# Optimization experiments

Measured on AMD Instinct MI355X. Metric: run time of the kernel, lower is better.

Reference implementation:

```python
import jax, jax.numpy as jnp
import numpy as np

RES, GATE, SKIP, K, DIL, CIN = 128, 256, 128, 3, 2, 80
PAD = (K - 1) * DIL


def _wn(v, g):
    # weight_norm: w = g * v / ||v||, norm over all dims except dim 0 (out_channels)
    norm = jnp.sqrt(jnp.sum(v * v, axis=(1, 2), keepdims=True))
    return v * (g.reshape(-1, 1, 1) / norm)


def setup_inputs() -> dict:
    key = jax.random.key(0)
    ks = jax.random.split(key, 12)
    s = lambda *sh: 1.0 / np.sqrt(np.prod(sh[1:]))
    d = {
        "x": jax.random.normal(ks[0], (8, RES, 32768), dtype=jnp.float32),
        "condition": jax.random.normal(ks[1], (8, CIN, 32768), dtype=jnp.float32),
        "conv_v": jax.random.normal(ks[2], (GATE, RES, K), dtype=jnp.float32) * s(GATE, RES, K),
        "conv_g": jnp.ones((GATE,), dtype=jnp.float32),
        "conv_b": jnp.zeros((GATE,), dtype=jnp.float32),
        "lc_v": jax.random.normal(ks[3], (GATE, CIN, 1), dtype=jnp.float32) * s(GATE, CIN, 1),
        "lc_g": jnp.ones((GATE,), dtype=jnp.float32),
        "skip_v": jax.random.normal(ks[4], (SKIP, GATE // 2, 1), dtype=jnp.float32) * s(SKIP, GATE // 2, 1),
        "skip_g": jnp.ones((SKIP,), dtype=jnp.float32),
        "skip_b": jnp.zeros((SKIP,), dtype=jnp.float32),
        "out_v": jax.random.normal(ks[5], (RES, GATE // 2, 1), dtype=jnp.float32) * s(RES, GATE // 2, 1),
        "out_g": jnp.ones((RES,), dtype=jnp.float32),
        "out_b": jnp.zeros((RES,), dtype=jnp.float32),
    }
    return d


def reference(x, condition, conv_v, conv_g, conv_b, lc_v, lc_g,
              skip_v, skip_g, skip_b, out_v, out_g, out_b):
    residual = x
    w = _wn(conv_v, conv_g)  # [GATE, RES, K]
    # torch pads symmetrically then slices [:, :, :-PAD]; equivalent to left-only pad
    h = jax.lax.conv_general_dilated(
        x, w, window_strides=(1,), padding=[(PAD, 0)], rhs_dilation=(DIL,),
        dimension_numbers=("NCH", "OIH", "NCH"))
    h = h + conv_b[None, :, None]  # [B, GATE, T]
    a, b = jnp.split(h, 2, axis=1)
    lc_w = _wn(lc_v, lc_g)[:, :, 0]  # [GATE, CIN]
    c = jnp.einsum("oc,bct->bot", lc_w, condition)
    ca, cb = jnp.split(c, 2, axis=1)
    g = jnp.tanh(a + ca) * jax.nn.sigmoid(b + cb)  # [B, GATE//2, T]
    skip_w = _wn(skip_v, skip_g)[:, :, 0]
    s = jnp.einsum("oc,bct->bot", skip_w, g) + skip_b[None, :, None]
    out_w = _wn(out_v, out_g)[:, :, 0]
    o = jnp.einsum("oc,bct->bot", out_w, g) + out_b[None, :, None]
    return (o + residual, s)
```

## Files before the change

### kernel.cpp

```cpp
#include <hip/hip_runtime.h>
#include <hip/hip_bf16.h>

#define B_N   8
#define T_N   32768
#define RESC  128
#define GATEC 256
#define CINC  80
#define CINP  96
#define NT    64
#define HALO  4
#define XROWS 68
#define XSTR  136
#define CSTR  96
#define HSTR  136

#define AP1_ELEMS (16*12*512)
#define AP2_ELEMS (16*3*512)
#define AP3_ELEMS (16*4*512)

#define OFF_S ((size_t)B_N * RESC * T_N)

typedef __attribute__((ext_vector_type(8))) short short8;
typedef __attribute__((ext_vector_type(4))) float f32x4;

__device__ __forceinline__ ushort f2bf(float f) {
  union { float f; unsigned int u; } c; c.f = f;
  unsigned int u = c.u;
  u += 0x7fffu + ((u >> 16) & 1u);
  return (ushort)(u >> 16);
}
__device__ __forceinline__ float bf2f(ushort s) {
  union { unsigned int u; float f; } c; c.u = ((unsigned int)s) << 16;
  return c.f;
}

__global__ __launch_bounds__(256) void wn_pack_kernel(
    const float* __restrict__ conv_v, const float* __restrict__ conv_g,
    const float* __restrict__ lc_v,  const float* __restrict__ lc_g,
    const float* __restrict__ skip_v,const float* __restrict__ skip_g,
    const float* __restrict__ out_v, const float* __restrict__ out_g,
    ushort* __restrict__ Ap1, ushort* __restrict__ Ap2, ushort* __restrict__ Ap3) {
  const int o   = blockIdx.x;
  const int tid = threadIdx.x;
  const int mtg = o >> 4, r = o & 15;
  __shared__ float red[256];

  float s = 0.f;
  for (int e = tid; e < RESC * 3; e += 256) { float v = conv_v[o * RESC * 3 + e]; s += v * v; }
  red[tid] = s; __syncthreads();
  for (int off = 128; off > 0; off >>= 1) { if (tid < off) red[tid] += red[tid + off]; __syncthreads(); }
  const float csc = conv_g[o] / sqrtf(red[0]);
  __syncthreads();
  for (int e = tid; e < 384; e += 256) {
    const int ks = e >> 5, q = (e >> 3) & 3, j = e & 7;
    const int tap = ks >> 2, ci = (ks & 3) * 32 + q * 8 + j;
    Ap1[((mtg * 12 + ks) * 64 + q * 16 + r) * 8 + j] = f2bf(conv_v[(o * RESC + ci) * 3 + tap] * csc);
  }

  s = 0.f;
  for (int e = tid; e < CINC; e += 256) { float v = lc_v[o * CINC + e]; s += v * v; }
  red[tid] = s; __syncthreads();
  for (int off = 128; off > 0; off >>= 1) { if (tid < off) red[tid] += red[tid + off]; __syncthreads(); }
  const float lsc = lc_g[o] / sqrtf(red[0]);
  __syncthreads();
  for (int e = tid; e < CINP; e += 256) {
    const int ks = e >> 5, q = (e >> 3) & 3, j = e & 7;
    const float wv = (e < CINC) ? lc_v[o * CINC + e] * lsc : 0.f;
    Ap2[((mtg * 3 + ks) * 64 + q * 16 + r) * 8 + j] = f2bf(wv);
  }

  const float* vrow = (o < 128) ? (skip_v + o * 128) : (out_v + (o - 128) * 128);
  const float  gg   = (o < 128) ? skip_g[o] : out_g[o - 128];
  s = 0.f;
  for (int e = tid; e < 128; e += 256) { float v = vrow[e]; s += v * v; }
  red[tid] = s; __syncthreads();
  for (int off = 128; off > 0; off >>= 1) { if (tid < off) red[tid] += red[tid + off]; __syncthreads(); }
  const float ssc = gg / sqrtf(red[0]);
  for (int e = tid; e < 128; e += 256) {
    const int ks = e >> 5, q = (e >> 3) & 3, j = e & 7;
    Ap3[((mtg * 4 + ks) * 64 + q * 16 + r) * 8 + j] = f2bf(vrow[e] * ssc);
  }
}

__global__ __launch_bounds__(256) void fused_block_kernel(
    const float* __restrict__ x, const float* __restrict__ cond,
    const float* __restrict__ conv_b, const float* __restrict__ skip_b,
    const float* __restrict__ out_b,
    const ushort* __restrict__ Ap1, const ushort* __restrict__ Ap2,
    const ushort* __restrict__ Ap3,
    float* __restrict__ out) {
  const int tid  = threadIdx.x;
  const int w    = tid >> 6;
  const int lane = tid & 63;
  const int q    = lane >> 4;
  const int n    = lane & 15;
  const int blk  = blockIdx.x;
  const int b    = blk >> 9;
  const int t0   = (blk & 511) << 6;

  __shared__ ushort smem[17408];
  ushort* xs  = smem;
  ushort* cs  = smem + XROWS * XSTR;
  ushort* hsA = smem;
  ushort* hsB = smem + NT * HSTR;

  {
    const int g4 = tid >> 3;
    const int c0 = g4 << 2;
    const int tt = (tid & 7) << 3;
    const float* xp = x + ((size_t)b * RESC + c0) * T_N + t0 + tt;
    float va[4][8];
#pragma unroll
    for (int rr = 0; rr < 4; ++rr) {
      const float4* rp = (const float4*)(xp + (size_t)rr * T_N);
      const float4 a0 = rp[0], a1 = rp[1];
      va[rr][0] = a0.x; va[rr][1] = a0.y; va[rr][2] = a0.z; va[rr][3] = a0.w;
      va[rr][4] = a1.x; va[rr][5] = a1.y; va[rr][6] = a1.z; va[rr][7] = a1.w;
    }
#pragma unroll
    for (int ss = 0; ss < 8; ++ss) {
      const unsigned lo = (unsigned)f2bf(va[0][ss]) | ((unsigned)f2bf(va[1][ss]) << 16);
      const unsigned hi = (unsigned)f2bf(va[2][ss]) | ((unsigned)f2bf(va[3][ss]) << 16);
      *(uint2*)&xs[(HALO + tt + ss) * XSTR + c0] = make_uint2(lo, hi);
    }
  }
  if (tid < RESC) {
    float h0 = 0.f, h1 = 0.f, h2 = 0.f, h3 = 0.f;
    if (t0 > 0) {
      const float4 hv = *(const float4*)(x + ((size_t)b * RESC + tid) * T_N + t0 - 4);
      h0 = hv.x; h1 = hv.y; h2 = hv.z; h3 = hv.w;
    }
    xs[0 * XSTR + tid] = f2bf(h0);
    xs[1 * XSTR + tid] = f2bf(h1);
    xs[2 * XSTR + tid] = f2bf(h2);
    xs[3 * XSTR + tid] = f2bf(h3);
  }
  if (tid < 160) {
    const int g4 = tid >> 3;
    const int c0 = g4 << 2;
    const int tt = (tid & 7) << 3;
    const float* cp = cond + ((size_t)b * CINC + c0) * T_N + t0 + tt;
    float va[4][8];
#pragma unroll
    for (int rr = 0; rr < 4; ++rr) {
      const float4* rp = (const float4*)(cp + (size_t)rr * T_N);
      const float4 a0 = rp[0], a1 = rp[1];
      va[rr][0] = a0.x; va[rr][1] = a0.y; va[rr][2] = a0.z; va[rr][3] = a0.w;
      va[rr][4] = a1.x; va[rr][5] = a1.y; va[rr][6] = a1.z; va[rr][7] = a1.w;
    }
#pragma unroll
    for (int ss = 0; ss < 8; ++ss) {
      const unsigned lo = (unsigned)f2bf(va[0][ss]) | ((unsigned)f2bf(va[1][ss]) << 16);
      const unsigned hi = (unsigned)f2bf(va[2][ss]) | ((unsigned)f2bf(va[3][ss]) << 16);
      *(uint2*)&cs[(tt + ss) * CSTR + c0] = make_uint2(lo, hi);
    }
  } else {
    const int e0 = tid - 160;
    for (int z = e0; z < 512; z += 96) {
      const int t = z >> 3, cp2 = z & 7;
      *(unsigned int*)&cs[t * CSTR + CINC + cp2 * 2] = 0u;
    }
  }
  __syncthreads();

  f32x4 acc[4][4];
#pragma unroll
  for (int mt = 0; mt < 4; ++mt) {
    const float4 cb = *(const float4*)(conv_b + w * 64 + mt * 16 + q * 4);
#pragma unroll
    for (int nt = 0; nt < 4; ++nt) acc[mt][nt] = (f32x4){cb.x, cb.y, cb.z, cb.w};
  }
#pragma unroll
  for (int ks = 0; ks < 12; ++ks) {
    const int tap = ks >> 2;
    const int cb2 = (ks & 3) << 5;
    short8 af[4], bfr[4];
#pragma unroll
    for (int mt = 0; mt < 4; ++mt)
      af[mt] = *(const short8*)(Ap1 + ((w * 4 + mt) * 12 + ks) * 512 + lane * 8);
#pragma unroll
    for (int nt = 0; nt < 4; ++nt)
      bfr[nt] = *(const short8*)&xs[(nt * 16 + n + tap * 2) * XSTR + cb2 + q * 8];
#pragma unroll
    for (int mt = 0; mt < 4; ++mt)
#pragma unroll
      for (int nt = 0; nt < 4; ++nt)
        acc[mt][nt] = __builtin_amdgcn_mfma_f32_16x16x32_bf16(af[mt], bfr[nt], acc[mt][nt], 0, 0, 0);
  }
#pragma unroll
  for (int ks = 0; ks < 3; ++ks) {
    short8 af[4], bfr[4];
#pragma unroll
    for (int mt = 0; mt < 4; ++mt)
      af[mt] = *(const short8*)(Ap2 + ((w * 4 + mt) * 3 + ks) * 512 + lane * 8);
#pragma unroll
    for (int nt = 0; nt < 4; ++nt)
      bfr[nt] = *(const short8*)&cs[(nt * 16 + n) * CSTR + ks * 32 + q * 8];
#pragma unroll
    for (int mt = 0; mt < 4; ++mt)
#pragma unroll
      for (int nt = 0; nt < 4; ++nt)
        acc[mt][nt] = __builtin_amdgcn_mfma_f32_16x16x32_bf16(af[mt], bfr[nt], acc[mt][nt], 0, 0, 0);
  }
  __syncthreads();

  const int colbase = (w & 1) << 6;
  {
    ushort* hdst = (w < 2) ? hsA : hsB;
#pragma unroll
    for (int mt = 0; mt < 4; ++mt)
#pragma unroll
      for (int nt = 0; nt < 4; ++nt) {
        const f32x4 v = acc[mt][nt];
        float r0, r1, r2, r3;
        if (w < 2) {
          r0 = 1.f - 2.f / (__expf(2.f * v[0]) + 1.f);
          r1 = 1.f - 2.f / (__expf(2.f * v[1]) + 1.f);
          r2 = 1.f - 2.f / (__expf(2.f * v[2]) + 1.f);
          r3 = 1.f - 2.f / (__expf(2.f * v[3]) + 1.f);
        } else {
          r0 = 1.f / (1.f + __expf(-v[0]));
          r1 = 1.f / (1.f + __expf(-v[1]));
          r2 = 1.f / (1.f + __expf(-v[2]));
          r3 = 1.f / (1.f + __expf(-v[3]));
        }
        const unsigned lo = (unsigned)f2bf(r0) | ((unsigned)f2bf(r1) << 16);
        const unsigned hi = (unsigned)f2bf(r2) | ((unsigned)f2bf(r3) << 16);
        *(uint2*)&hdst[(nt * 16 + n) * HSTR + colbase + mt * 16 + q * 4] = make_uint2(lo, hi);
      }
  }
  __syncthreads();

  {
    const int prow = tid >> 2;
    const int pc0  = (tid & 3) << 5;
#pragma unroll
    for (int s2 = 0; s2 < 8; ++s2) {
      const int col = pc0 + (s2 << 2);
      const uint2 ua = *(uint2*)&hsA[prow * HSTR + col];
      const uint2 ub = *(uint2*)&hsB[prow * HSTR + col];
      const float a0 = bf2f((ushort)ua.x), a1 = bf2f((ushort)(ua.x >> 16));
      const float a2 = bf2f((ushort)ua.y), a3 = bf2f((ushort)(ua.y >> 16));
      const float b0 = bf2f((ushort)ub.x), b1 = bf2f((ushort)(ub.x >> 16));
      const float b2 = bf2f((ushort)ub.y), b3 = bf2f((ushort)(ub.y >> 16));
      const unsigned lo = (unsigned)f2bf(a0 * b0) | ((unsigned)f2bf(a1 * b1) << 16);
      const unsigned hi = (unsigned)f2bf(a2 * b2) | ((unsigned)f2bf(a3 * b3) << 16);
      *(uint2*)&hsA[prow * HSTR + col] = make_uint2(lo, hi);
    }
  }
  __syncthreads();

  {
    const float* bias = (w < 2) ? skip_b : out_b;
#pragma unroll
    for (int mt = 0; mt < 4; ++mt) {
      const float4 bb = *(const float4*)(bias + colbase + mt * 16 + q * 4);
#pragma unroll
      for (int nt = 0; nt < 4; ++nt) acc[mt][nt] = (f32x4){bb.x, bb.y, bb.z, bb.w};
    }
#pragma unroll
    for (int ks = 0; ks < 4; ++ks) {
      short8 af[4], bfr[4];
#pragma unroll
      for (int mt = 0; mt < 4; ++mt)
        af[mt] = *(const short8*)(Ap3 + ((w * 4 + mt) * 4 + ks) * 512 + lane * 8);
#pragma unroll
      for (int nt = 0; nt < 4; ++nt)
        bfr[nt] = *(const short8*)&hsA[(nt * 16 + n) * HSTR + ks * 32 + q * 8];
#pragma unroll
      for (int mt = 0; mt < 4; ++mt)
#pragma unroll
        for (int nt = 0; nt < 4; ++nt)
          acc[mt][nt] = __builtin_amdgcn_mfma_f32_16x16x32_bf16(af[mt], bfr[nt], acc[mt][nt], 0, 0, 0);
    }
  }

#pragma unroll
  for (int mt = 0; mt < 4; ++mt)
#pragma unroll
    for (int nt = 0; nt < 4; ++nt) {
      const int ch = colbase + mt * 16 + q * 4;
      const int t  = t0 + nt * 16 + n;
      const f32x4 v = acc[mt][nt];
      if (w < 2) {
        float* dst = out + OFF_S + ((size_t)(b * RESC + ch)) * T_N + t;
#pragma unroll
        for (int i = 0; i < 4; ++i) dst[(size_t)i * T_N] = v[i];
      } else {
        const float* xr = x + ((size_t)(b * RESC + ch)) * T_N + t;
        float* dst = out + ((size_t)(b * RESC + ch)) * T_N + t;
#pragma unroll
        for (int i = 0; i < 4; ++i) dst[(size_t)i * T_N] = v[i] + xr[(size_t)i * T_N];
      }
    }
}

extern "C" void kernel_launch(void* const* d_in, const int* in_sizes, int n_in,
                              void* d_out, int out_size, void* d_ws, size_t ws_size,
                              hipStream_t stream) {
  const float* x      = (const float*)d_in[0];
  const float* cond   = (const float*)d_in[1];
  const float* conv_v = (const float*)d_in[2];
  const float* conv_g = (const float*)d_in[3];
  const float* conv_b = (const float*)d_in[4];
  const float* lc_v   = (const float*)d_in[5];
  const float* lc_g   = (const float*)d_in[6];
  const float* skip_v = (const float*)d_in[7];
  const float* skip_g = (const float*)d_in[8];
  const float* skip_b = (const float*)d_in[9];
  const float* out_v  = (const float*)d_in[10];
  const float* out_g  = (const float*)d_in[11];
  const float* out_b  = (const float*)d_in[12];

  ushort* Ap1 = (ushort*)d_ws;
  ushort* Ap2 = Ap1 + AP1_ELEMS;
  ushort* Ap3 = Ap2 + AP2_ELEMS;

  hipLaunchKernelGGL(wn_pack_kernel, dim3(256), dim3(256), 0, stream,
                     conv_v, conv_g, lc_v, lc_g, skip_v, skip_g, out_v, out_g,
                     Ap1, Ap2, Ap3);
  hipLaunchKernelGGL(fused_block_kernel, dim3(4096), dim3(256), 0, stream,
                     x, cond, conv_b, skip_b, out_b, Ap1, Ap2, Ap3, (float*)d_out);
}
```

Baseline: 509.4 us.

## Gate tanh/sigmoid in registers and swap operands for time-contiguous output stores

Each wave now computes matching tanh and sigmoid channel halves (aa/ab accumulators) so the gate product is formed in registers. This removes the separate shared-memory elementwise multiply pass and one barrier. The final GEMM swaps operand roles so each lane holds four consecutive time steps, which allows float4 global stores and residual loads instead of strided scalar accesses. Input staging is reorganized to use packed bf16 conversion with 16-byte LDS stores, and the shared-memory footprint is reduced. The cost is some added address arithmetic.

```diff
diff --git a/kernel.cpp b/kernel.cpp
--- a/kernel.cpp
+++ b/kernel.cpp
@@ -6,13 +6,11 @@
 #define RESC  128
 #define GATEC 256
 #define CINC  80
-#define CINP  96
 #define NT    64
 #define HALO  4
 #define XROWS 68
 #define XSTR  136
-#define CSTR  96
-#define HSTR  136
+#define CSTR  104
 
 #define AP1_ELEMS (16*12*512)
 #define AP2_ELEMS (16*3*512)
@@ -29,9 +27,9 @@
   u += 0x7fffu + ((u >> 16) & 1u);
   return (ushort)(u >> 16);
 }
-__device__ __forceinline__ float bf2f(ushort s) {
-  union { unsigned int u; float f; } c; c.u = ((unsigned int)s) << 16;
-  return c.f;
+__device__ __forceinline__ unsigned pkbf(float a, float b) {
+  __hip_bfloat162 h = __float22bfloat162_rn(float2{a, b});
+  unsigned u; __builtin_memcpy(&u, &h, 4); return u;
 }
 
 __global__ __launch_bounds__(256) void wn_pack_kernel(
@@ -63,7 +61,7 @@
   for (int off = 128; off > 0; off >>= 1) { if (tid < off) red[tid] += red[tid + off]; __syncthreads(); }
   const float lsc = lc_g[o] / sqrtf(red[0]);
   __syncthreads();
-  for (int e = tid; e < CINP; e += 256) {
+  for (int e = tid; e < 96; e += 256) {
     const int ks = e >> 5, q = (e >> 3) & 3, j = e & 7;
     const float wv = (e < CINC) ? lc_v[o * CINC + e] * lsc : 0.f;
     Ap2[((mtg * 3 + ks) * 64 + q * 16 + r) * 8 + j] = f2bf(wv);
@@ -98,30 +96,27 @@
   const int b    = blk >> 9;
   const int t0   = (blk & 511) << 6;
 
-  __shared__ ushort smem[17408];
-  ushort* xs  = smem;
-  ushort* cs  = smem + XROWS * XSTR;
-  ushort* hsA = smem;
-  ushort* hsB = smem + NT * HSTR;
+  __shared__ ushort smem[XROWS * XSTR + NT * CSTR];
+  ushort* xs = smem;
+  ushort* cs = smem + XROWS * XSTR;
+  ushort* gs = smem;
 
   {
-    const int g4 = tid >> 3;
-    const int c0 = g4 << 2;
-    const int tt = (tid & 7) << 3;
+    const int c0 = (tid & 15) << 3;
+    const int tt = (tid >> 4) << 2;
     const float* xp = x + ((size_t)b * RESC + c0) * T_N + t0 + tt;
-    float va[4][8];
-#pragma unroll
-    for (int rr = 0; rr < 4; ++rr) {
-      const float4* rp = (const float4*)(xp + (size_t)rr * T_N);
-      const float4 a0 = rp[0], a1 = rp[1];
-      va[rr][0] = a0.x; va[rr][1] = a0.y; va[rr][2] = a0.z; va[rr][3] = a0.w;
-      va[rr][4] = a1.x; va[rr][5] = a1.y; va[rr][6] = a1.z; va[rr][7] = a1.w;
-    }
-#pragma unroll
-    for (int ss = 0; ss < 8; ++ss) {
-      const unsigned lo = (unsigned)f2bf(va[0][ss]) | ((unsigned)f2bf(va[1][ss]) << 16);
-      const unsigned hi = (unsigned)f2bf(va[2][ss]) | ((unsigned)f2bf(va[3][ss]) << 16);
-      *(uint2*)&xs[(HALO + tt + ss) * XSTR + c0] = make_uint2(lo, hi);
+    float4 va[8];
+#pragma unroll
+    for (int rr = 0; rr < 8; ++rr) va[rr] = *(const float4*)(xp + (size_t)rr * T_N);
+    const float* vf = (const float*)va;
+#pragma unroll
+    for (int i = 0; i < 4; ++i) {
+      uint4 pkd;
+      pkd.x = pkbf(vf[0 * 4 + i], vf[1 * 4 + i]);
+      pkd.y = pkbf(vf[2 * 4 + i], vf[3 * 4 + i]);
+      pkd.z = pkbf(vf[4 * 4 + i], vf[5 * 4 + i]);
+      pkd.w = pkbf(vf[6 * 4 + i], vf[7 * 4 + i]);
+      *(uint4*)&xs[(HALO + tt + i) * XSTR + c0] = pkd;
     }
   }
   if (tid < RESC) {
@@ -135,164 +130,148 @@
     xs[2 * XSTR + tid] = f2bf(h2);
     xs[3 * XSTR + tid] = f2bf(h3);
   }
-  if (tid < 160) {
-    const int g4 = tid >> 3;
-    const int c0 = g4 << 2;
-    const int tt = (tid & 7) << 3;
-    const float* cp = cond + ((size_t)b * CINC + c0) * T_N + t0 + tt;
-    float va[4][8];
-#pragma unroll
-    for (int rr = 0; rr < 4; ++rr) {
-      const float4* rp = (const float4*)(cp + (size_t)rr * T_N);
-      const float4 a0 = rp[0], a1 = rp[1];
-      va[rr][0] = a0.x; va[rr][1] = a0.y; va[rr][2] = a0.z; va[rr][3] = a0.w;
-      va[rr][4] = a1.x; va[rr][5] = a1.y; va[rr][6] = a1.z; va[rr][7] = a1.w;
-    }
-#pragma unroll
-    for (int ss = 0; ss < 8; ++ss) {
-      const unsigned lo = (unsigned)f2bf(va[0][ss]) | ((unsigned)f2bf(va[1][ss]) << 16);
-      const unsigned hi = (unsigned)f2bf(va[2][ss]) | ((unsigned)f2bf(va[3][ss]) << 16);
-      *(uint2*)&cs[(tt + ss) * CSTR + c0] = make_uint2(lo, hi);
-    }
-  } else {
-    const int e0 = tid - 160;
-    for (int z = e0; z < 512; z += 96) {
-      const int t = z >> 3, cp2 = z & 7;
-      *(unsigned int*)&cs[t * CSTR + CINC + cp2 * 2] = 0u;
-    }
-  }
-  __syncthreads();
-
-  f32x4 acc[4][4];
-#pragma unroll
-  for (int mt = 0; mt < 4; ++mt) {
-    const float4 cb = *(const float4*)(conv_b + w * 64 + mt * 16 + q * 4);
-#pragma unroll
-    for (int nt = 0; nt < 4; ++nt) acc[mt][nt] = (f32x4){cb.x, cb.y, cb.z, cb.w};
+  if (tid < 192) {
+    const int cb = tid % 12;
+    const int tq = tid / 12;
+    const int c0 = cb << 3;
+    const int tt = tq << 2;
+    if (cb < 10) {
+      const float* cp = cond + ((size_t)b * CINC + c0) * T_N + t0 + tt;
+      float4 va[8];
+#pragma unroll
+      for (int rr = 0; rr < 8; ++rr) va[rr] = *(const float4*)(cp + (size_t)rr * T_N);
+      const float* vf = (const float*)va;
+#pragma unroll
+      for (int i = 0; i < 4; ++i) {
+        uint4 pkd;
+        pkd.x = pkbf(vf[0 * 4 + i], vf[1 * 4 + i]);
+        pkd.y = pkbf(vf[2 * 4 + i], vf[3 * 4 + i]);
+        pkd.z = pkbf(vf[4 * 4 + i], vf[5 * 4 + i]);
+        pkd.w = pkbf(vf[6 * 4 + i], vf[7 * 4 + i]);
+        *(uint4*)&cs[(tt + i) * CSTR + c0] = pkd;
+      }
+    } else {
+#pragma unroll
+      for (int i = 0; i < 4; ++i)
+        *(uint4*)&cs[(tt + i) * CSTR + c0] = make_uint4(0, 0, 0, 0);
+    }
+  }
+  __syncthreads();
+
+  f32x4 aa[2][4], ab[2][4];
+#pragma unroll
+  for (int mt = 0; mt < 2; ++mt) {
+    const float4 ca = *(const float4*)(conv_b + w * 32 + mt * 16 + q * 4);
+    const float4 cb2 = *(const float4*)(conv_b + 128 + w * 32 + mt * 16 + q * 4);
+#pragma unroll
+    for (int nt = 0; nt < 4; ++nt) {
+      aa[mt][nt] = (f32x4){ca.x, ca.y, ca.z, ca.w};
+      ab[mt][nt] = (f32x4){cb2.x, cb2.y, cb2.z, cb2.w};
+    }
   }
 #pragma unroll
   for (int ks = 0; ks < 12; ++ks) {
     const int tap = ks >> 2;
-    const int cb2 = (ks & 3) << 5;
-    short8 af[4], bfr[4];
+    const int kc  = (ks & 3) << 5;
+    short8 afa[2], afb[2], bfr[4];
+#pragma unroll
+    for (int mt = 0; mt < 2; ++mt) {
+      afa[mt] = *(const short8*)(Ap1 + (((w * 2 + mt) * 12 + ks) << 9) + lane * 8);
+      afb[mt] = *(const short8*)(Ap1 + (((8 + w * 2 + mt) * 12 + ks) << 9) + lane * 8);
+    }
+#pragma unroll
+    for (int nt = 0; nt < 4; ++nt)
+      bfr[nt] = *(const short8*)&xs[(nt * 16 + n + tap * 2) * XSTR + kc + q * 8];
+#pragma unroll
+    for (int mt = 0; mt < 2; ++mt)
+#pragma unroll
+      for (int nt = 0; nt < 4; ++nt) {
+        aa[mt][nt] = __builtin_amdgcn_mfma_f32_16x16x32_bf16(afa[mt], bfr[nt], aa[mt][nt], 0, 0, 0);
+        ab[mt][nt] = __builtin_amdgcn_mfma_f32_16x16x32_bf16(afb[mt], bfr[nt], ab[mt][nt], 0, 0, 0);
+      }
+  }
+#pragma unroll
+  for (int ks = 0; ks < 3; ++ks) {
+    short8 afa[2], afb[2], bfr[4];
+#pragma unroll
+    for (int mt = 0; mt < 2; ++mt) {
+      afa[mt] = *(const short8*)(Ap2 + (((w * 2 + mt) * 3 + ks) << 9) + lane * 8);
+      afb[mt] = *(const short8*)(Ap2 + (((8 + w * 2 + mt) * 3 + ks) << 9) + lane * 8);
+    }
+#pragma unroll
+    for (int nt = 0; nt < 4; ++nt)
+      bfr[nt] = *(const short8*)&cs[(nt * 16 + n) * CSTR + (ks << 5) + q * 8];
+#pragma unroll
+    for (int mt = 0; mt < 2; ++mt)
+#pragma unroll
+      for (int nt = 0; nt < 4; ++nt) {
+        aa[mt][nt] = __builtin_amdgcn_mfma_f32_16x16x32_bf16(afa[mt], bfr[nt], aa[mt][nt], 0, 0, 0);
+        ab[mt][nt] = __builtin_amdgcn_mfma_f32_16x16x32_bf16(afb[mt], bfr[nt], ab[mt][nt], 0, 0, 0);
+      }
+  }
+  __syncthreads();
+
+#pragma unroll
+  for (int mt = 0; mt < 2; ++mt)
+#pragma unroll
+    for (int nt = 0; nt < 4; ++nt) {
+      const f32x4 va_ = aa[mt][nt];
+      const f32x4 vb_ = ab[mt][nt];
+      float g4[4];
+#pragma unroll
+      for (int i = 0; i < 4; ++i) {
+        const float th = 1.f - 2.f / (__expf(2.f * va_[i]) + 1.f);
+        const float sg = 1.f / (1.f + __expf(-vb_[i]));
+        g4[i] = th * sg;
+      }
+      const uint2 pkd = make_uint2(pkbf(g4[0], g4[1]), pkbf(g4[2], g4[3]));
+      *(uint2*)&gs[(nt * 16 + n) * XSTR + w * 32 + mt * 16 + q * 4] = pkd;
+    }
+  __syncthreads();
+
+  {
+    const int chbase = (w & 1) << 6;
+    const float* bias = (w < 2) ? skip_b : out_b;
+    f32x4 acc[4][4];
+#pragma unroll
+    for (int nt = 0; nt < 4; ++nt) {
+      const float bv = bias[chbase + nt * 16 + n];
+#pragma unroll
+      for (int mt = 0; mt < 4; ++mt) acc[mt][nt] = (f32x4){bv, bv, bv, bv};
+    }
+#pragma unroll
+    for (int ks = 0; ks < 4; ++ks) {
+      short8 ag[4], bw[4];
+#pragma unroll
+      for (int mt = 0; mt < 4; ++mt)
+        ag[mt] = *(const short8*)&gs[(mt * 16 + n) * XSTR + (ks << 5) + q * 8];
+#pragma unroll
+      for (int nt = 0; nt < 4; ++nt)
+        bw[nt] = *(const short8*)(Ap3 + (((w * 4 + nt) * 4 + ks) << 9) + lane * 8);
+#pragma unroll
+      for (int mt = 0; mt < 4; ++mt)
+#pragma unroll
+        for (int nt = 0; nt < 4; ++nt)
+          acc[mt][nt] = __builtin_amdgcn_mfma_f32_16x16x32_bf16(ag[mt], bw[nt], acc[mt][nt], 0, 0, 0);
+    }
+
 #pragma unroll
     for (int mt = 0; mt < 4; ++mt)
-      af[mt] = *(const short8*)(Ap1 + ((w * 4 + mt) * 12 + ks) * 512 + lane * 8);
-#pragma unroll
-    for (int nt = 0; nt < 4; ++nt)
-      bfr[nt] = *(const short8*)&xs[(nt * 16 + n + tap * 2) * XSTR + cb2 + q * 8];
-#pragma unroll
-    for (int mt = 0; mt < 4; ++mt)
-#pragma unroll
-      for (int nt = 0; nt < 4; ++nt)
-        acc[mt][nt] = __builtin_amdgcn_mfma_f32_16x16x32_bf16(af[mt], bfr[nt], acc[mt][nt], 0, 0, 0);
-  }
-#pragma unroll
-  for (int ks = 0; ks < 3; ++ks) {
-    short8 af[4], bfr[4];
-#pragma unroll
-    for (int mt = 0; mt < 4; ++mt)
-      af[mt] = *(const short8*)(Ap2 + ((w * 4 + mt) * 3 + ks) * 512 + lane * 8);
-#pragma unroll
-    for (int nt = 0; nt < 4; ++nt)
-      bfr[nt] = *(const short8*)&cs[(nt * 16 + n) * CSTR + ks * 32 + q * 8];
-#pragma unroll
-    for (int mt = 0; mt < 4; ++mt)
-#pragma unroll
-      for (int nt = 0; nt < 4; ++nt)
-        acc[mt][nt] = __builtin_amdgcn_mfma_f32_16x16x32_bf16(af[mt], bfr[nt], acc[mt][nt], 0, 0, 0);
-  }
-  __syncthreads();
-
-  const int colbase = (w & 1) << 6;
-  {
-    ushort* hdst = (w < 2) ? hsA : hsB;
-#pragma unroll
-    for (int mt = 0; mt < 4; ++mt)
 #pragma unroll
       for (int nt = 0; nt < 4; ++nt) {
+        const int ch = chbase + nt * 16 + n;
+        const int t  = t0 + mt * 16 + q * 4;
         const f32x4 v = acc[mt][nt];
-        float r0, r1, r2, r3;
         if (w < 2) {
-          r0 = 1.f - 2.f / (__expf(2.f * v[0]) + 1.f);
-          r1 = 1.f - 2.f / (__expf(2.f * v[1]) + 1.f);
-          r2 = 1.f - 2.f / (__expf(2.f * v[2]) + 1.f);
-          r3 = 1.f - 2.f / (__expf(2.f * v[3]) + 1.f);
+          *(float4*)(out + OFF_S + ((size_t)(b * RESC + ch)) * T_N + t) =
+              make_float4(v[0], v[1], v[2], v[3]);
         } else {
-          r0 = 1.f / (1.f + __expf(-v[0]));
-          r1 = 1.f / (1.f + __expf(-v[1]));
-          r2 = 1.f / (1.f + __expf(-v[2]));
-          r3 = 1.f / (1.f + __expf(-v[3]));
+          const float4 xr = *(const float4*)(x + ((size_t)(b * RESC + ch)) * T_N + t);
+          *(float4*)(out + ((size_t)(b * RESC + ch)) * T_N + t) =
+              make_float4(v[0] + xr.x, v[1] + xr.y, v[2] + xr.z, v[3] + xr.w);
         }
-        const unsigned lo = (unsigned)f2bf(r0) | ((unsigned)f2bf(r1) << 16);
-        const unsigned hi = (unsigned)f2bf(r2) | ((unsigned)f2bf(r3) << 16);
-        *(uint2*)&hdst[(nt * 16 + n) * HSTR + colbase + mt * 16 + q * 4] = make_uint2(lo, hi);
-      }
-  }
-  __syncthreads();
-
-  {
-    const int prow = tid >> 2;
-    const int pc0  = (tid & 3) << 5;
-#pragma unroll
-    for (int s2 = 0; s2 < 8; ++s2) {
-      const int col = pc0 + (s2 << 2);
-      const uint2 ua = *(uint2*)&hsA[prow * HSTR + col];
-      const uint2 ub = *(uint2*)&hsB[prow * HSTR + col];
-      const float a0 = bf2f((ushort)ua.x), a1 = bf2f((ushort)(ua.x >> 16));
-      const float a2 = bf2f((ushort)ua.y), a3 = bf2f((ushort)(ua.y >> 16));
-      const float b0 = bf2f((ushort)ub.x), b1 = bf2f((ushort)(ub.x >> 16));
-      const float b2 = bf2f((ushort)ub.y), b3 = bf2f((ushort)(ub.y >> 16));
-      const unsigned lo = (unsigned)f2bf(a0 * b0) | ((unsigned)f2bf(a1 * b1) << 16);
-      const unsigned hi = (unsigned)f2bf(a2 * b2) | ((unsigned)f2bf(a3 * b3) << 16);
-      *(uint2*)&hsA[prow * HSTR + col] = make_uint2(lo, hi);
-    }
-  }
-  __syncthreads();
-
-  {
-    const float* bias = (w < 2) ? skip_b : out_b;
-#pragma unroll
-    for (int mt = 0; mt < 4; ++mt) {
-      const float4 bb = *(const float4*)(bias + colbase + mt * 16 + q * 4);
-#pragma unroll
-      for (int nt = 0; nt < 4; ++nt) acc[mt][nt] = (f32x4){bb.x, bb.y, bb.z, bb.w};
-    }
-#pragma unroll
-    for (int ks = 0; ks < 4; ++ks) {
-      short8 af[4], bfr[4];
-#pragma unroll
-      for (int mt = 0; mt < 4; ++mt)
-        af[mt] = *(const short8*)(Ap3 + ((w * 4 + mt) * 4 + ks) * 512 + lane * 8);
-#pragma unroll
-      for (int nt = 0; nt < 4; ++nt)
-        bfr[nt] = *(const short8*)&hsA[(nt * 16 + n) * HSTR + ks * 32 + q * 8];
-#pragma unroll
-      for (int mt = 0; mt < 4; ++mt)
-#pragma unroll
-        for (int nt = 0; nt < 4; ++nt)
-          acc[mt][nt] = __builtin_amdgcn_mfma_f32_16x16x32_bf16(af[mt], bfr[nt], acc[mt][nt], 0, 0, 0);
-    }
-  }
-
-#pragma unroll
-  for (int mt = 0; mt < 4; ++mt)
-#pragma unroll
-    for (int nt = 0; nt < 4; ++nt) {
-      const int ch = colbase + mt * 16 + q * 4;
-      const int t  = t0 + nt * 16 + n;
-      const f32x4 v = acc[mt][nt];
-      if (w < 2) {
-        float* dst = out + OFF_S + ((size_t)(b * RESC + ch)) * T_N + t;
-#pragma unroll
-        for (int i = 0; i < 4; ++i) dst[(size_t)i * T_N] = v[i];
-      } else {
-        const float* xr = x + ((size_t)(b * RESC + ch)) * T_N + t;
-        float* dst = out + ((size_t)(b * RESC + ch)) * T_N + t;
-#pragma unroll
-        for (int i = 0; i < 4; ++i) dst[(size_t)i * T_N] = v[i] + xr[(size_t)i * T_N];
-      }
-    }
+      }
+  }
 }
 
 extern "C" void kernel_launch(void* const* d_in, const int* in_sizes, int n_in,
```

Result: slower. 546.0 us (+7.2%).
